# Kernel tuning notes

Measured on AMD Instinct MI355X. Metric: run time of the kernel, lower is better.

The kernel has to match this reference:

```python
import jax, jax.numpy as jnp
import numpy as np


def setup_inputs() -> dict:
    key = jax.random.key(0)
    ks = jax.random.split(key, 7)
    b, c, h, w = 4, 256, 64, 64
    ci = c // 2
    inp = {
        "x0": jax.random.normal(ks[0], (b, 2 * c, h, w), dtype=jnp.float32),
        "x": jax.random.normal(ks[1], (b, c, h, w), dtype=jnp.float32),
        "x_dsm": jax.random.normal(ks[2], (b, c, h, w), dtype=jnp.float32),
        # 1x1 conv weights, stored as [out_ch, in_ch]
        "w_phi": jax.random.normal(ks[3], (ci, c), dtype=jnp.float32) * 0.02,
        "w_theta": jax.random.normal(ks[4], (ci, c), dtype=jnp.float32) * 0.02,
        "w_g": jax.random.normal(ks[5], (c, 2 * c), dtype=jnp.float32) * 0.02,
        "w_mask": jax.random.normal(ks[6], (2 * c, c), dtype=jnp.float32) * 0.02,
    }
    return inp


def reference(x0, x, x_dsm, w_phi, w_theta, w_g, w_mask):
    b, c, h, w = x.shape
    ci = c // 2
    n = h * w
    # 1x1 convs as channel matmuls
    phi = jnp.einsum('oc,bchw->bohw', w_phi, x).reshape(b, ci, n)            # [b, ci, N]
    theta = jnp.einsum('oc,bchw->bohw', w_theta, x_dsm).reshape(b, ci, n)    # [b, ci, N]
    theta = theta.transpose(0, 2, 1)                                         # [b, N, ci]
    g = jnp.einsum('oc,bchw->bohw', w_g, x0).reshape(b, c, n).transpose(0, 2, 1)  # [b, N, c]
    scores = jnp.matmul(theta, phi)                                          # [b, N, N]
    # NOTE: original uses nn.Softmax(dim=1) -> normalize over the FIRST N axis
    attn = jax.nn.softmax(scores, axis=1)
    out = jnp.matmul(attn, g)                                                # [b, N, c]
    out = out.transpose(0, 2, 1).reshape(b, c, h, w)
    mask = jnp.einsum('oc,bchw->bohw', w_mask, out)                          # [b, 2c, h, w]
    return mask + x0
```

## Files before the change

kernel.cpp:

```cpp
#include <hip/hip_runtime.h>
#include <math.h>

#define NB 4
#define NC 256
#define NCI 128
#define NC2 512
#define NPOS 4096
#define ISPLIT 8

using bf16x8 = __attribute__((ext_vector_type(8))) short;
using f32x4  = __attribute__((ext_vector_type(4))) float;

__device__ inline unsigned short f2bf(float f) {
  unsigned int u = __float_as_uint(f);
  u = (u + 0x7fffu + ((u >> 16) & 1u)) >> 16;
  return (unsigned short)u;
}
__device__ inline float bf2f(short s) {
  return __uint_as_float(((unsigned int)(unsigned short)s) << 16);
}

__global__ void k_cast4(const float* __restrict__ s0, short* __restrict__ d0, int n0,
                        const float* __restrict__ s1, short* __restrict__ d1, int n1,
                        const float* __restrict__ s2, short* __restrict__ d2, int n2,
                        const float* __restrict__ s3, short* __restrict__ d3, int n3) {
  int i = blockIdx.x * 256 + threadIdx.x;
  if (i < n0) { d0[i] = (short)f2bf(s0[i]); return; } i -= n0;
  if (i < n1) { d1[i] = (short)f2bf(s1[i]); return; } i -= n1;
  if (i < n2) { d2[i] = (short)f2bf(s2[i]); return; } i -= n2;
  if (i < n3) { d3[i] = (short)f2bf(s3[i]); }
}

__global__ __launch_bounds__(256) void k_tcast(
    const float* __restrict__ in, short* __restrict__ out,
    int R, int C, size_t inBs, size_t outBs) {
  __shared__ float t[64][65];
  const int tid = threadIdx.x;
  const int r0 = blockIdx.y * 64, c0 = blockIdx.x * 64, b = blockIdx.z;
  {
    int r = tid >> 2, cc = (tid & 3) * 16;
    const float* ib = in + (size_t)b * inBs + (size_t)(r0 + r) * C + c0 + cc;
#pragma unroll
    for (int i = 0; i < 4; ++i) {
      float4 v = *(const float4*)(ib + i * 4);
      t[r][cc + i * 4 + 0] = v.x; t[r][cc + i * 4 + 1] = v.y;
      t[r][cc + i * 4 + 2] = v.z; t[r][cc + i * 4 + 3] = v.w;
    }
  }
  __syncthreads();
  {
    int c = tid >> 2, rr = (tid & 3) * 16;
    __align__(16) short v[16];
#pragma unroll
    for (int i = 0; i < 16; ++i) v[i] = (short)f2bf(t[rr + i][c]);
    short* ob = out + (size_t)b * outBs + (size_t)(c0 + c) * R + r0 + rr;
    *(int4*)(ob) = *(const int4*)(v);
    *(int4*)(ob + 8) = *(const int4*)(v + 8);
  }
}

__global__ __launch_bounds__(256) void k_tcast2(
    const float* __restrict__ inA, const float* __restrict__ inB,
    short* __restrict__ out, int R, int C, size_t inBs, size_t outBs) {
  __shared__ float t[64][65];
  const int tid = threadIdx.x;
  const int r0 = blockIdx.y * 64, c0 = blockIdx.x * 64, b = blockIdx.z;
  {
    int r = tid >> 2, cc = (tid & 3) * 16;
    size_t base = (size_t)b * inBs + (size_t)(r0 + r) * C + c0 + cc;
#pragma unroll
    for (int i = 0; i < 4; ++i) {
      float4 va = *(const float4*)(inA + base + i * 4);
      float4 vb = *(const float4*)(inB + base + i * 4);
      t[r][cc + i * 4 + 0] = va.x + vb.x; t[r][cc + i * 4 + 1] = va.y + vb.y;
      t[r][cc + i * 4 + 2] = va.z + vb.z; t[r][cc + i * 4 + 3] = va.w + vb.w;
    }
  }
  __syncthreads();
  {
    int c = tid >> 2, rr = (tid & 3) * 16;
    __align__(16) short v[16];
#pragma unroll
    for (int i = 0; i < 16; ++i) v[i] = (short)f2bf(t[rr + i][c]);
    short* ob = out + (size_t)b * outBs + (size_t)(c0 + c) * R + r0 + rr;
    *(int4*)(ob) = *(const int4*)(v);
    *(int4*)(ob + 8) = *(const int4*)(v + 8);
  }
}

template<bool OUT_BF16, bool HAS_RES>
__global__ __launch_bounds__(256, 2) void k_gemm(
    const short* __restrict__ A, const short* __restrict__ B,
    void* __restrict__ outv, const float* __restrict__ res,
    int K, int sN, size_t aBs, size_t bBs, size_t oBs) {
  __shared__ short As[2][64 * 64];
  __shared__ short Bs_[2][64 * 64];
  const int tid = threadIdx.x, lane = tid & 63, w = tid >> 6;
  const int x = lane & 15, q = lane >> 4;
  const int wm = (w & 1) * 32, wn = (w >> 1) * 32;
  const int n0 = blockIdx.x * 64, m0 = blockIdx.y * 64, b = blockIdx.z;
  const short* Ab = A + (size_t)b * aBs + (size_t)m0 * K;
  const short* Bb = B + (size_t)b * bBs + (size_t)n0 * K;
  const int r = tid >> 2, cth = tid & 3;
  f32x4 acc[2][2];
  acc[0][0] = acc[0][1] = acc[1][0] = acc[1][1] = (f32x4){0.f, 0.f, 0.f, 0.f};
  int4 ra[2], rb[2];
  const int NK = K >> 6;
#define GLOAD(kt)                                                              \
  { _Pragma("unroll") for (int i = 0; i < 2; ++i) {                            \
      ra[i] = *(const int4*)(Ab + (size_t)r * K + (kt) * 64 + (cth + i * 4) * 8); \
      rb[i] = *(const int4*)(Bb + (size_t)r * K + (kt) * 64 + (cth + i * 4) * 8); } }
#define GWRITE(buf)                                                            \
  { _Pragma("unroll") for (int i = 0; i < 2; ++i) {                            \
      *(int4*)(&As[buf][r * 64 + (((cth + i * 4) ^ (r & 7)) * 8)]) = ra[i];    \
      *(int4*)(&Bs_[buf][r * 64 + (((cth + i * 4) ^ (r & 7)) * 8)]) = rb[i]; } }
  GLOAD(0); GWRITE(0); __syncthreads();
  int cur = 0;
  for (int kt = 0; kt < NK; ++kt) {
    if (kt + 1 < NK) GLOAD(kt + 1);
    bf16x8 af[2][2], bfr[2][2];
#pragma unroll
    for (int ms = 0; ms < 2; ++ms) {
      int rowm = wm + ms * 16 + x;
#pragma unroll
      for (int ks = 0; ks < 2; ++ks)
        af[ms][ks] = *(const bf16x8*)(&As[cur][rowm * 64 + (((ks * 4 + q) ^ (rowm & 7)) * 8)]);
    }
#pragma unroll
    for (int ns = 0; ns < 2; ++ns) {
      int rown = wn + ns * 16 + x;
#pragma unroll
      for (int ks = 0; ks < 2; ++ks)
        bfr[ns][ks] = *(const bf16x8*)(&Bs_[cur][rown * 64 + (((ks * 4 + q) ^ (rown & 7)) * 8)]);
    }
#pragma unroll
    for (int ms = 0; ms < 2; ++ms)
#pragma unroll
      for (int ns = 0; ns < 2; ++ns)
#pragma unroll
        for (int ks = 0; ks < 2; ++ks)
          acc[ms][ns] = __builtin_amdgcn_mfma_f32_16x16x32_bf16(
              af[ms][ks], bfr[ns][ks], acc[ms][ns], 0, 0, 0);
    if (kt + 1 < NK) GWRITE(cur ^ 1);
    __syncthreads();
    cur ^= 1;
  }
#pragma unroll
  for (int ms = 0; ms < 2; ++ms)
#pragma unroll
    for (int ns = 0; ns < 2; ++ns) {
      int n = n0 + wn + ns * 16 + x;
      int m = m0 + wm + ms * 16 + q * 4;
      size_t off = (size_t)b * oBs + (size_t)n * sN + m;
      if (OUT_BF16) {
        __align__(8) short pv[4];
#pragma unroll
        for (int j = 0; j < 4; ++j) pv[j] = (short)f2bf(acc[ms][ns][j]);
        *(uint2*)((short*)outv + off) = *(const uint2*)pv;
      } else {
        float4 v = {acc[ms][ns][0], acc[ms][ns][1], acc[ms][ns][2], acc[ms][ns][3]};
        if (HAS_RES) {
          float4 rv = *(const float4*)(res + off);
          v.x += rv.x; v.y += rv.y; v.z += rv.z; v.w += rv.w;
        }
        *(float4*)((float*)outv + off) = v;
      }
    }
#undef GLOAD
#undef GWRITE
}

__global__ __launch_bounds__(256, 4) void k_lsum(
    const short* __restrict__ phiB, const short* __restrict__ thetaB,
    float* __restrict__ plsum) {
  __shared__ short thT[2][64 * 128];
  const int tid = threadIdx.x, lane = tid & 63, w = tid >> 6;
  const int x = lane & 15, q = lane >> 4;
  const int j0 = blockIdx.x * 64, iy = blockIdx.y, b = blockIdx.z;
  const short* phb = phiB + (size_t)b * NPOS * NCI;
  const short* thb = thetaB + (size_t)b * NPOS * NCI + (size_t)iy * (NPOS / ISPLIT) * NCI;
  bf16x8 af[4];
  {
    const short* pr = phb + (size_t)(j0 + w * 16 + x) * NCI;
#pragma unroll
    for (int kk = 0; kk < 4; ++kk) af[kk] = *(const bf16x8*)(pr + kk * 32 + q * 8);
  }
  float lsum[4] = {0.f, 0.f, 0.f, 0.f};
  int4 rt[4];
  const int NIT = NPOS / ISPLIT / 64;
#define LSUM_LOAD(it)                                                         \
  { _Pragma("unroll") for (int r = 0; r < 4; ++r) {                           \
      int s = tid + r * 256; int row = s >> 4, c = s & 15;                    \
      rt[r] = *(const int4*)(thb + (size_t)((it) * 64 + row) * NCI + c * 8); } }
#define LSUM_WRITE(buf)                                                       \
  { _Pragma("unroll") for (int r = 0; r < 4; ++r) {                           \
      int s = tid + r * 256; int row = s >> 4, c = s & 15;                    \
      *(int4*)(&thT[buf][row * 128 + ((c ^ (row & 7)) * 8)]) = rt[r]; } }
  LSUM_LOAD(0); LSUM_WRITE(0); __syncthreads();
  int cur = 0;
  for (int it = 0; it < NIT; ++it) {
    if (it + 1 < NIT) LSUM_LOAD(it + 1);
#pragma unroll
    for (int ii = 0; ii < 4; ++ii) {
      f32x4 s = {0.f, 0.f, 0.f, 0.f};
      int row = ii * 16 + x;
      int sw = row & 7;
#pragma unroll
      for (int kk = 0; kk < 4; ++kk) {
        bf16x8 bfv = *(const bf16x8*)(&thT[cur][row * 128 + (((kk * 4 + q) ^ sw) * 8)]);
        s = __builtin_amdgcn_mfma_f32_16x16x32_bf16(af[kk], bfv, s, 0, 0, 0);
      }
#pragma unroll
      for (int r = 0; r < 4; ++r) lsum[r] += __expf(s[r]);
    }
    if (it + 1 < NIT) LSUM_WRITE(cur ^ 1);
    __syncthreads();
    cur ^= 1;
  }
#pragma unroll
  for (int m = 1; m < 16; m <<= 1)
#pragma unroll
    for (int r = 0; r < 4; ++r) lsum[r] += __shfl_xor(lsum[r], m);
  if (x == 0) {
#pragma unroll
    for (int r = 0; r < 4; ++r)
      plsum[((size_t)(b * ISPLIT + iy) << 12) + j0 + w * 16 + 4 * q + r] = lsum[r];
  }
#undef LSUM_LOAD
#undef LSUM_WRITE
}

__global__ void k_lcomb(const float* __restrict__ plsum, float* __restrict__ linv) {
  int i = blockIdx.x * 256 + threadIdx.x;
  int b = i >> 12, j = i & (NPOS - 1);
  float s = 0.f;
#pragma unroll
  for (int t = 0; t < ISPLIT; ++t) s += plsum[((size_t)(b * ISPLIT + t) << 12) + j];
  linv[i] = 1.0f / s;
}

__global__ void k_scale_g(short* __restrict__ gB, const float* __restrict__ linv) {
  size_t e = ((size_t)blockIdx.x * 256 + threadIdx.x) * 8;
  int b = (int)(e >> 20);
  int p = (int)(e & (NPOS - 1));
  __align__(16) short v[8];
  *(int4*)v = *(const int4*)(gB + e);
  const float* lv = linv + ((size_t)b << 12) + p;
#pragma unroll
  for (int k = 0; k < 8; ++k) v[k] = (short)f2bf(bf2f(v[k]) * lv[k]);
  *(int4*)(gB + e) = *(const int4*)v;
}

__global__ __launch_bounds__(256, 2) void k_attn(
    const short* __restrict__ phiB, const short* __restrict__ thetaB,
    const short* __restrict__ gB, float* __restrict__ omidP) {
  __shared__ short phiT[2][32 * 128];
  __shared__ short gT[2][256 * 32];
  __shared__ short pT[4][16 * 32];
  const int tid = threadIdx.x, lane = tid & 63, w = tid >> 6;
  const int x = lane & 15, q = lane >> 4;
  const int i0 = blockIdx.x * 64, jh = blockIdx.y, b = blockIdx.z;
  const short* phb = phiB + (size_t)b * NPOS * NCI;
  const short* thb = thetaB + (size_t)b * NPOS * NCI;
  const short* gb = gB + (size_t)b * NC * NPOS;
  float* om = omidP + ((size_t)(jh * NB + b)) * NC * NPOS;

  bf16x8 tf[4];
  {
    const short* tr = thb + (size_t)(i0 + w * 16 + x) * NCI;
#pragma unroll
    for (int kk = 0; kk < 4; ++kk) tf[kk] = *(const bf16x8*)(tr + kk * 32 + q * 8);
  }
  f32x4 acc[16];
#pragma unroll
  for (int i = 0; i < 16; ++i) acc[i] = (f32x4){0.f, 0.f, 0.f, 0.f};

  const int sgx = (x & 3) ^ ((x >> 2) & 1);
  int4 rphi[2], rg[4];
  const int NT = 64;
  const int jbase = jh * 64;
#define ATTN_LOAD(jt)                                                          \
  { _Pragma("unroll") for (int r = 0; r < 2; ++r) {                            \
      int s = tid + r * 256; int row = s >> 4, c = s & 15;                     \
      rphi[r] = *(const int4*)(phb + (size_t)((jbase + (jt)) * 32 + row) * NCI + c * 8); } \
    _Pragma("unroll") for (int r = 0; r < 4; ++r) {                            \
      int s = tid + r * 256; int cc = s >> 2, c4 = s & 3;                      \
      rg[r] = *(const int4*)(gb + (size_t)cc * NPOS + (jbase + (jt)) * 32 + c4 * 8); } }
#define ATTN_WRITE(buf)                                                        \
  { _Pragma("unroll") for (int r = 0; r < 2; ++r) {                            \
      int s = tid + r * 256; int row = s >> 4, c = s & 15;                     \
      *(int4*)(&phiT[buf][row * 128 + ((c ^ (row & 7)) * 8)]) = rphi[r]; }     \
    _Pragma("unroll") for (int r = 0; r < 4; ++r) {                            \
      int s = tid + r * 256; int cc = s >> 2, c4 = s & 3;                      \
      int sw = (cc & 3) ^ ((cc >> 2) & 1);                                     \
      *(int4*)(&gT[buf][cc * 32 + ((c4 ^ sw) * 8)]) = rg[r]; } }
  ATTN_LOAD(0); ATTN_WRITE(0); __syncthreads();
  int cur = 0;
  for (int jt = 0; jt < NT; ++jt) {
    if (jt + 1 < NT) ATTN_LOAD(jt + 1);
    {
      const short* PH = &phiT[cur][0];
      const short* GT = &gT[cur][0];
      short* PW = &pT[w][0];
#pragma unroll
      for (int jsub = 0; jsub < 2; ++jsub) {
        f32x4 s = {0.f, 0.f, 0.f, 0.f};
        int row = jsub * 16 + x;
        int sw = row & 7;
#pragma unroll
        for (int kk = 0; kk < 4; ++kk) {
          bf16x8 a = *(const bf16x8*)(PH + row * 128 + (((kk * 4 + q) ^ sw) * 8));
          s = __builtin_amdgcn_mfma_f32_16x16x32_bf16(a, tf[kk], s, 0, 0, 0);
        }
        unsigned short p0 = f2bf(__expf(s[0]));
        unsigned short p1 = f2bf(__expf(s[1]));
        unsigned short p2 = f2bf(__expf(s[2]));
        unsigned short p3 = f2bf(__expf(s[3]));
        unsigned int lo = (unsigned int)p0 | ((unsigned int)p1 << 16);
        unsigned int hi = (unsigned int)p2 | ((unsigned int)p3 << 16);
        int byteoff = (x * 64 + jsub * 32 + q * 8) ^ ((((x >> 1) & 3)) << 4);
        *(uint2*)((char*)PW + byteoff) = make_uint2(lo, hi);
      }
      {
        int c = q ^ ((x >> 1) & 3);
        bf16x8 ap = *(const bf16x8*)((const char*)PW + x * 64 + c * 16);
#pragma unroll
        for (int cf = 0; cf < 16; ++cf) {
          bf16x8 bg = *(const bf16x8*)(GT + (cf * 16 + x) * 32 + ((q ^ sgx) * 8));
          acc[cf] = __builtin_amdgcn_mfma_f32_16x16x32_bf16(ap, bg, acc[cf], 0, 0, 0);
        }
      }
    }
    if (jt + 1 < NT) ATTN_WRITE(cur ^ 1);
    __syncthreads();
    cur ^= 1;
  }
#pragma unroll
  for (int cf = 0; cf < 16; ++cf) {
    size_t o = (size_t)(cf * 16 + x) * NPOS + i0 + w * 16 + 4 * q;
    *reinterpret_cast<f32x4*>(&om[o]) = acc[cf];
  }
#undef ATTN_LOAD
#undef ATTN_WRITE
}

extern "C" void kernel_launch(void* const* d_in, const int* in_sizes, int n_in,
                              void* d_out, int out_size, void* d_ws, size_t ws_size,
                              hipStream_t stream) {
  (void)in_sizes; (void)n_in; (void)out_size; (void)ws_size;
  const float* x0      = (const float*)d_in[0];
  const float* x       = (const float*)d_in[1];
  const float* x_dsm   = (const float*)d_in[2];
  const float* w_phi   = (const float*)d_in[3];
  const float* w_theta = (const float*)d_in[4];
  const float* w_g     = (const float*)d_in[5];
  const float* w_mask  = (const float*)d_in[6];
  float* outp = (float*)d_out;

  short* sp = (short*)d_ws;
  short* wb_phi   = sp; sp += 32768;
  short* wb_theta = sp; sp += 32768;
  short* wb_g     = sp; sp += 131072;
  short* wb_mask  = sp; sp += 131072;
  short* xT   = sp; sp += (size_t)NB * NPOS * NC;
  short* xdT  = sp; sp += (size_t)NB * NPOS * NC;
  short* x0T  = sp; sp += (size_t)NB * NPOS * NC2;
  short* phiB   = sp; sp += (size_t)NB * NPOS * NCI;
  short* thetaB = sp; sp += (size_t)NB * NPOS * NCI;
  short* gBuf   = sp; sp += (size_t)NB * NC * NPOS;
  float* linv = (float*)sp; sp += 2 * (size_t)NB * NPOS;
  float* plsum = (float*)sp;
  float* omidP = (float*)xT;
  short* omidT = phiB;

  k_cast4<<<dim3(1280), 256, 0, stream>>>(w_phi, wb_phi, 32768,
                                          w_theta, wb_theta, 32768,
                                          w_g, wb_g, 131072,
                                          w_mask, wb_mask, 131072);

  k_tcast<<<dim3(64, 4, NB), 256, 0, stream>>>(x, xT, NC, NPOS,
      (size_t)NC * NPOS, (size_t)NPOS * NC);
  k_tcast<<<dim3(64, 4, NB), 256, 0, stream>>>(x_dsm, xdT, NC, NPOS,
      (size_t)NC * NPOS, (size_t)NPOS * NC);
  k_tcast<<<dim3(64, 8, NB), 256, 0, stream>>>(x0, x0T, NC2, NPOS,
      (size_t)NC2 * NPOS, (size_t)NPOS * NC2);

  k_gemm<true, false><<<dim3(64, 2, NB), 256, 0, stream>>>(
      wb_phi, xT, phiB, nullptr, NC, NCI, 0, (size_t)NPOS * NC, (size_t)NPOS * NCI);
  k_gemm<true, false><<<dim3(64, 2, NB), 256, 0, stream>>>(
      wb_theta, xdT, thetaB, nullptr, NC, NCI, 0, (size_t)NPOS * NC, (size_t)NPOS * NCI);
  k_gemm<true, false><<<dim3(4, 64, NB), 256, 0, stream>>>(
      x0T, wb_g, gBuf, nullptr, NC2, NPOS, (size_t)NPOS * NC2, 0, (size_t)NC * NPOS);

  k_lsum<<<dim3(NPOS / 64, ISPLIT, NB), 256, 0, stream>>>(phiB, thetaB, plsum);
  k_lcomb<<<dim3(NB * NPOS / 256), 256, 0, stream>>>(plsum, linv);
  k_scale_g<<<dim3(2048), 256, 0, stream>>>(gBuf, linv);

  k_attn<<<dim3(64, 2, NB), 256, 0, stream>>>(phiB, thetaB, gBuf, omidP);

  k_tcast2<<<dim3(64, 4, NB), 256, 0, stream>>>(omidP, omidP + (size_t)NB * NC * NPOS,
      omidT, NC, NPOS, (size_t)NC * NPOS, (size_t)NPOS * NC);

  k_gemm<false, true><<<dim3(8, 64, NB), 256, 0, stream>>>(
      omidT, wb_mask, outp, x0, NC, NPOS, (size_t)NPOS * NC, 0, (size_t)NC2 * NPOS);
}
```

Before: 255.3 us.

## Retile attention kernel across warps, split keys four ways, store bf16 partials

The attention kernel now has warps split the P computation by key half and query half, then share P through LDS. Each warp owns 64 output channels across all 64 queries, so each g fragment feeds four MFMAs instead of one. The key dimension is split four ways instead of two, which gives more blocks, and occupancy is raised to 3. Partial outputs are written as bf16 instead of fp32 and reduced by a new 4-way transpose-cast kernel. The costs are an extra barrier per tile and bf16 rounding of the partial sums.

```diff
diff --git a/kernel.cpp b/kernel.cpp
--- a/kernel.cpp
+++ b/kernel.cpp
@@ -59,22 +59,25 @@
   }
 }
 
-__global__ __launch_bounds__(256) void k_tcast2(
-    const float* __restrict__ inA, const float* __restrict__ inB,
-    short* __restrict__ out, int R, int C, size_t inBs, size_t outBs) {
+__global__ __launch_bounds__(256) void k_tcast4(
+    const short* __restrict__ inP, short* __restrict__ out) {
   __shared__ float t[64][65];
   const int tid = threadIdx.x;
   const int r0 = blockIdx.y * 64, c0 = blockIdx.x * 64, b = blockIdx.z;
   {
     int r = tid >> 2, cc = (tid & 3) * 16;
-    size_t base = (size_t)b * inBs + (size_t)(r0 + r) * C + c0 + cc;
-#pragma unroll
-    for (int i = 0; i < 4; ++i) {
-      float4 va = *(const float4*)(inA + base + i * 4);
-      float4 vb = *(const float4*)(inB + base + i * 4);
-      t[r][cc + i * 4 + 0] = va.x + vb.x; t[r][cc + i * 4 + 1] = va.y + vb.y;
-      t[r][cc + i * 4 + 2] = va.z + vb.z; t[r][cc + i * 4 + 3] = va.w + vb.w;
-    }
+    float tacc[16] = {};
+#pragma unroll
+    for (int p = 0; p < 4; ++p) {
+      const short* ib = inP + ((size_t)p * NB + b) * NC * NPOS +
+                        (size_t)(r0 + r) * NPOS + c0 + cc;
+      bf16x8 a = *(const bf16x8*)(ib);
+      bf16x8 a2 = *(const bf16x8*)(ib + 8);
+#pragma unroll
+      for (int i = 0; i < 8; ++i) { tacc[i] += bf2f(a[i]); tacc[8 + i] += bf2f(a2[i]); }
+    }
+#pragma unroll
+    for (int i = 0; i < 16; ++i) t[r][cc + i] = tacc[i];
   }
   __syncthreads();
   {
@@ -82,7 +85,7 @@
     __align__(16) short v[16];
 #pragma unroll
     for (int i = 0; i < 16; ++i) v[i] = (short)f2bf(t[rr + i][c]);
-    short* ob = out + (size_t)b * outBs + (size_t)(c0 + c) * R + r0 + rr;
+    short* ob = out + (size_t)b * (size_t)NPOS * NC + (size_t)(c0 + c) * NC + r0 + rr;
     *(int4*)(ob) = *(const int4*)(v);
     *(int4*)(ob + 8) = *(const int4*)(v + 8);
   }
@@ -251,41 +254,46 @@
   *(int4*)(gB + e) = *(const int4*)v;
 }
 
-__global__ __launch_bounds__(256, 2) void k_attn(
+__global__ __launch_bounds__(256, 3) void k_attn(
     const short* __restrict__ phiB, const short* __restrict__ thetaB,
-    const short* __restrict__ gB, float* __restrict__ omidP) {
+    const short* __restrict__ gB, short* __restrict__ omidP) {
   __shared__ short phiT[2][32 * 128];
   __shared__ short gT[2][256 * 32];
-  __shared__ short pT[4][16 * 32];
+  __shared__ short pT[64 * 32];
   const int tid = threadIdx.x, lane = tid & 63, w = tid >> 6;
   const int x = lane & 15, q = lane >> 4;
-  const int i0 = blockIdx.x * 64, jh = blockIdx.y, b = blockIdx.z;
+  const int jsub = w & 1, ih = w >> 1;
+  const int i0 = blockIdx.x * 64, jq = blockIdx.y, b = blockIdx.z;
   const short* phb = phiB + (size_t)b * NPOS * NCI;
   const short* thb = thetaB + (size_t)b * NPOS * NCI;
   const short* gb = gB + (size_t)b * NC * NPOS;
-  float* om = omidP + ((size_t)(jh * NB + b)) * NC * NPOS;
-
-  bf16x8 tf[4];
-  {
-    const short* tr = thb + (size_t)(i0 + w * 16 + x) * NCI;
-#pragma unroll
-    for (int kk = 0; kk < 4; ++kk) tf[kk] = *(const bf16x8*)(tr + kk * 32 + q * 8);
-  }
-  f32x4 acc[16];
-#pragma unroll
-  for (int i = 0; i < 16; ++i) acc[i] = (f32x4){0.f, 0.f, 0.f, 0.f};
-
+  short* om = omidP + ((size_t)(jq * NB + b)) * NC * NPOS;
+
+  bf16x8 tf[2][4];
+#pragma unroll
+  for (int f = 0; f < 2; ++f) {
+    const short* tr = thb + (size_t)(i0 + ih * 32 + f * 16 + x) * NCI;
+#pragma unroll
+    for (int kk = 0; kk < 4; ++kk) tf[f][kk] = *(const bf16x8*)(tr + kk * 32 + q * 8);
+  }
+  f32x4 acc[4][4];
+#pragma unroll
+  for (int i = 0; i < 4; ++i)
+#pragma unroll
+    for (int j = 0; j < 4; ++j) acc[i][j] = (f32x4){0.f, 0.f, 0.f, 0.f};
+
+  const int sx = (x >> 1) & 3;
   const int sgx = (x & 3) ^ ((x >> 2) & 1);
   int4 rphi[2], rg[4];
-  const int NT = 64;
-  const int jbase = jh * 64;
+  const int NT = 32;
+  const int JT0 = jq * 32;
 #define ATTN_LOAD(jt)                                                          \
   { _Pragma("unroll") for (int r = 0; r < 2; ++r) {                            \
       int s = tid + r * 256; int row = s >> 4, c = s & 15;                     \
-      rphi[r] = *(const int4*)(phb + (size_t)((jbase + (jt)) * 32 + row) * NCI + c * 8); } \
+      rphi[r] = *(const int4*)(phb + (size_t)((JT0 + (jt)) * 32 + row) * NCI + c * 8); } \
     _Pragma("unroll") for (int r = 0; r < 4; ++r) {                            \
       int s = tid + r * 256; int cc = s >> 2, c4 = s & 3;                      \
-      rg[r] = *(const int4*)(gb + (size_t)cc * NPOS + (jbase + (jt)) * 32 + c4 * 8); } }
+      rg[r] = *(const int4*)(gb + (size_t)cc * NPOS + (JT0 + (jt)) * 32 + c4 * 8); } }
 #define ATTN_WRITE(buf)                                                        \
   { _Pragma("unroll") for (int r = 0; r < 2; ++r) {                            \
       int s = tid + r * 256; int row = s >> 4, c = s & 15;                     \
@@ -298,19 +306,18 @@
   int cur = 0;
   for (int jt = 0; jt < NT; ++jt) {
     if (jt + 1 < NT) ATTN_LOAD(jt + 1);
+    const short* PH = &phiT[cur][0];
+    const short* GT = &gT[cur][0];
     {
-      const short* PH = &phiT[cur][0];
-      const short* GT = &gT[cur][0];
-      short* PW = &pT[w][0];
-#pragma unroll
-      for (int jsub = 0; jsub < 2; ++jsub) {
+      int row = jsub * 16 + x;
+      int swr = row & 7;
+#pragma unroll
+      for (int f = 0; f < 2; ++f) {
         f32x4 s = {0.f, 0.f, 0.f, 0.f};
-        int row = jsub * 16 + x;
-        int sw = row & 7;
 #pragma unroll
         for (int kk = 0; kk < 4; ++kk) {
-          bf16x8 a = *(const bf16x8*)(PH + row * 128 + (((kk * 4 + q) ^ sw) * 8));
-          s = __builtin_amdgcn_mfma_f32_16x16x32_bf16(a, tf[kk], s, 0, 0, 0);
+          bf16x8 a = *(const bf16x8*)(PH + row * 128 + (((kk * 4 + q) ^ swr) * 8));
+          s = __builtin_amdgcn_mfma_f32_16x16x32_bf16(a, tf[f][kk], s, 0, 0, 0);
         }
         unsigned short p0 = f2bf(__expf(s[0]));
         unsigned short p1 = f2bf(__expf(s[1]));
@@ -318,17 +325,24 @@
         unsigned short p3 = f2bf(__expf(s[3]));
         unsigned int lo = (unsigned int)p0 | ((unsigned int)p1 << 16);
         unsigned int hi = (unsigned int)p2 | ((unsigned int)p3 << 16);
-        int byteoff = (x * 64 + jsub * 32 + q * 8) ^ ((((x >> 1) & 3)) << 4);
-        *(uint2*)((char*)PW + byteoff) = make_uint2(lo, hi);
+        int irow = ih * 32 + f * 16 + x;
+        int byteoff = (irow * 64 + jsub * 32 + q * 8) ^ (sx << 4);
+        *(uint2*)((char*)pT + byteoff) = make_uint2(lo, hi);
       }
-      {
-        int c = q ^ ((x >> 1) & 3);
-        bf16x8 ap = *(const bf16x8*)((const char*)PW + x * 64 + c * 16);
-#pragma unroll
-        for (int cf = 0; cf < 16; ++cf) {
-          bf16x8 bg = *(const bf16x8*)(GT + (cf * 16 + x) * 32 + ((q ^ sgx) * 8));
-          acc[cf] = __builtin_amdgcn_mfma_f32_16x16x32_bf16(ap, bg, acc[cf], 0, 0, 0);
-        }
+    }
+    __syncthreads();
+    {
+      bf16x8 ap[4];
+#pragma unroll
+      for (int f = 0; f < 4; ++f)
+        ap[f] = *(const bf16x8*)((const char*)pT + (f * 16 + x) * 64 + ((q ^ sx) * 16));
+#pragma unroll
+      for (int cfl = 0; cfl < 4; ++cfl) {
+        int row = w * 64 + cfl * 16 + x;
+        bf16x8 bg = *(const bf16x8*)(GT + row * 32 + ((q ^ sgx) * 8));
+#pragma unroll
+        for (int f = 0; f < 4; ++f)
+          acc[f][cfl] = __builtin_amdgcn_mfma_f32_16x16x32_bf16(ap[f], bg, acc[f][cfl], 0, 0, 0);
       }
     }
     if (jt + 1 < NT) ATTN_WRITE(cur ^ 1);
@@ -336,10 +350,15 @@
     cur ^= 1;
   }
 #pragma unroll
-  for (int cf = 0; cf < 16; ++cf) {
-    size_t o = (size_t)(cf * 16 + x) * NPOS + i0 + w * 16 + 4 * q;
-    *reinterpret_cast<f32x4*>(&om[o]) = acc[cf];
-  }
+  for (int f = 0; f < 4; ++f)
+#pragma unroll
+    for (int cfl = 0; cfl < 4; ++cfl) {
+      __align__(8) short pv[4];
+#pragma unroll
+      for (int j = 0; j < 4; ++j) pv[j] = (short)f2bf(acc[f][cfl][j]);
+      size_t o = (size_t)(w * 64 + cfl * 16 + x) * NPOS + i0 + f * 16 + 4 * q;
+      *(uint2*)(om + o) = *(const uint2*)pv;
+    }
 #undef ATTN_LOAD
 #undef ATTN_WRITE
 }
@@ -370,7 +389,7 @@
   short* gBuf   = sp; sp += (size_t)NB * NC * NPOS;
   float* linv = (float*)sp; sp += 2 * (size_t)NB * NPOS;
   float* plsum = (float*)sp;
-  float* omidP = (float*)xT;
+  short* omidP = xT;
   short* omidT = phiB;
 
   k_cast4<<<dim3(1280), 256, 0, stream>>>(w_phi, wb_phi, 32768,
@@ -396,10 +415,9 @@
   k_lcomb<<<dim3(NB * NPOS / 256), 256, 0, stream>>>(plsum, linv);
   k_scale_g<<<dim3(2048), 256, 0, stream>>>(gBuf, linv);
 
-  k_attn<<<dim3(64, 2, NB), 256, 0, stream>>>(phiB, thetaB, gBuf, omidP);
-
-  k_tcast2<<<dim3(64, 4, NB), 256, 0, stream>>>(omidP, omidP + (size_t)NB * NC * NPOS,
-      omidT, NC, NPOS, (size_t)NC * NPOS, (size_t)NPOS * NC);
+  k_attn<<<dim3(64, 4, NB), 256, 0, stream>>>(phiB, thetaB, gBuf, omidP);
+
+  k_tcast4<<<dim3(64, 4, NB), 256, 0, stream>>>(omidP, omidT);
 
   k_gemm<false, true><<<dim3(8, 64, NB), 256, 0, stream>>>(
       omidT, wb_mask, outp, x0, NC, NPOS, (size_t)NPOS * NC, 0, (size_t)NC2 * NPOS);
```

After: 427.9 us. +67.6%, slower.

## Fuse softmax normalization into attention, share P tile across waves, bf16 partials

Applied to the files above, without the earlier changes.

Merges the three input transpose-cast launches into one kernel and removes the separate g-scaling pass by multiplying exp(scores) by the column inverse sums inside the attention kernel. The attention kernel now writes all four waves' P tiles into one shared tile, synchronizes, and has each wave compute a 64x64 output block (4x4 MFMA tiles), so each g fragment is reused across four P fragments instead of one. Partial outputs are stored as bf16 rather than fp32, which halves the write and read traffic into the transpose-add kernel. The cost is an extra barrier per j-tile, extra linv loads in the inner loop, and reduced precision of the partial sums.

```diff
diff --git a/kernel.cpp b/kernel.cpp
--- a/kernel.cpp
+++ b/kernel.cpp
@@ -31,15 +31,21 @@
   if (i < n3) { d3[i] = (short)f2bf(s3[i]); }
 }
 
-__global__ __launch_bounds__(256) void k_tcast(
-    const float* __restrict__ in, short* __restrict__ out,
-    int R, int C, size_t inBs, size_t outBs) {
+__global__ __launch_bounds__(256) void k_tcast_all(
+    const float* __restrict__ x, const float* __restrict__ xdsm,
+    const float* __restrict__ x0, short* __restrict__ xT,
+    short* __restrict__ xdT, short* __restrict__ x0T) {
   __shared__ float t[64][65];
   const int tid = threadIdx.x;
-  const int r0 = blockIdx.y * 64, c0 = blockIdx.x * 64, b = blockIdx.z;
+  const int y = blockIdx.y, c0 = blockIdx.x * 64, b = blockIdx.z;
+  const float* in; short* out; int R, r0;
+  if (y < 4)      { in = x;    out = xT;  R = NC;  r0 = y * 64; }
+  else if (y < 8) { in = xdsm; out = xdT; R = NC;  r0 = (y - 4) * 64; }
+  else            { in = x0;   out = x0T; R = NC2; r0 = (y - 8) * 64; }
+  const size_t inBs = (size_t)R * NPOS, outBs = (size_t)NPOS * R;
   {
     int r = tid >> 2, cc = (tid & 3) * 16;
-    const float* ib = in + (size_t)b * inBs + (size_t)(r0 + r) * C + c0 + cc;
+    const float* ib = in + (size_t)b * inBs + (size_t)(r0 + r) * NPOS + c0 + cc;
 #pragma unroll
     for (int i = 0; i < 4; ++i) {
       float4 v = *(const float4*)(ib + i * 4);
@@ -60,20 +66,22 @@
 }
 
 __global__ __launch_bounds__(256) void k_tcast2(
-    const float* __restrict__ inA, const float* __restrict__ inB,
-    short* __restrict__ out, int R, int C, size_t inBs, size_t outBs) {
+    const short* __restrict__ inA, const short* __restrict__ inB,
+    short* __restrict__ out) {
   __shared__ float t[64][65];
   const int tid = threadIdx.x;
   const int r0 = blockIdx.y * 64, c0 = blockIdx.x * 64, b = blockIdx.z;
   {
     int r = tid >> 2, cc = (tid & 3) * 16;
-    size_t base = (size_t)b * inBs + (size_t)(r0 + r) * C + c0 + cc;
-#pragma unroll
-    for (int i = 0; i < 4; ++i) {
-      float4 va = *(const float4*)(inA + base + i * 4);
-      float4 vb = *(const float4*)(inB + base + i * 4);
-      t[r][cc + i * 4 + 0] = va.x + vb.x; t[r][cc + i * 4 + 1] = va.y + vb.y;
-      t[r][cc + i * 4 + 2] = va.z + vb.z; t[r][cc + i * 4 + 3] = va.w + vb.w;
+    size_t base = (size_t)b * NC * NPOS + (size_t)(r0 + r) * NPOS + c0 + cc;
+    bf16x8 a0 = *(const bf16x8*)(inA + base);
+    bf16x8 a1 = *(const bf16x8*)(inA + base + 8);
+    bf16x8 b0 = *(const bf16x8*)(inB + base);
+    bf16x8 b1 = *(const bf16x8*)(inB + base + 8);
+#pragma unroll
+    for (int i = 0; i < 8; ++i) {
+      t[r][cc + i] = bf2f(a0[i]) + bf2f(b0[i]);
+      t[r][cc + 8 + i] = bf2f(a1[i]) + bf2f(b1[i]);
     }
   }
   __syncthreads();
@@ -82,7 +90,7 @@
     __align__(16) short v[16];
 #pragma unroll
     for (int i = 0; i < 16; ++i) v[i] = (short)f2bf(t[rr + i][c]);
-    short* ob = out + (size_t)b * outBs + (size_t)(c0 + c) * R + r0 + rr;
+    short* ob = out + (size_t)b * (size_t)NPOS * NC + (size_t)(c0 + c) * NC + r0 + rr;
     *(int4*)(ob) = *(const int4*)(v);
     *(int4*)(ob + 8) = *(const int4*)(v + 8);
   }
@@ -239,31 +247,21 @@
   linv[i] = 1.0f / s;
 }
 
-__global__ void k_scale_g(short* __restrict__ gB, const float* __restrict__ linv) {
-  size_t e = ((size_t)blockIdx.x * 256 + threadIdx.x) * 8;
-  int b = (int)(e >> 20);
-  int p = (int)(e & (NPOS - 1));
-  __align__(16) short v[8];
-  *(int4*)v = *(const int4*)(gB + e);
-  const float* lv = linv + ((size_t)b << 12) + p;
-#pragma unroll
-  for (int k = 0; k < 8; ++k) v[k] = (short)f2bf(bf2f(v[k]) * lv[k]);
-  *(int4*)(gB + e) = *(const int4*)v;
-}
-
 __global__ __launch_bounds__(256, 2) void k_attn(
     const short* __restrict__ phiB, const short* __restrict__ thetaB,
-    const short* __restrict__ gB, float* __restrict__ omidP) {
+    const short* __restrict__ gB, const float* __restrict__ linv,
+    short* __restrict__ omidP) {
   __shared__ short phiT[2][32 * 128];
   __shared__ short gT[2][256 * 32];
-  __shared__ short pT[4][16 * 32];
+  __shared__ short pT[64 * 32];
   const int tid = threadIdx.x, lane = tid & 63, w = tid >> 6;
   const int x = lane & 15, q = lane >> 4;
   const int i0 = blockIdx.x * 64, jh = blockIdx.y, b = blockIdx.z;
   const short* phb = phiB + (size_t)b * NPOS * NCI;
   const short* thb = thetaB + (size_t)b * NPOS * NCI;
   const short* gb = gB + (size_t)b * NC * NPOS;
-  float* om = omidP + ((size_t)(jh * NB + b)) * NC * NPOS;
+  const float* lvb = linv + ((size_t)b << 12);
+  short* om = omidP + ((size_t)(jh * NB + b)) * NC * NPOS;
 
   bf16x8 tf[4];
   {
@@ -271,10 +269,13 @@
 #pragma unroll
     for (int kk = 0; kk < 4; ++kk) tf[kk] = *(const bf16x8*)(tr + kk * 32 + q * 8);
   }
-  f32x4 acc[16];
-#pragma unroll
-  for (int i = 0; i < 16; ++i) acc[i] = (f32x4){0.f, 0.f, 0.f, 0.f};
-
+  f32x4 acc[4][4];
+#pragma unroll
+  for (int i = 0; i < 4; ++i)
+#pragma unroll
+    for (int j = 0; j < 4; ++j) acc[i][j] = (f32x4){0.f, 0.f, 0.f, 0.f};
+
+  const int px = (x >> 1) & 3;
   const int sgx = (x & 3) ^ ((x >> 2) & 1);
   int4 rphi[2], rg[4];
   const int NT = 64;
@@ -300,8 +301,6 @@
     if (jt + 1 < NT) ATTN_LOAD(jt + 1);
     {
       const short* PH = &phiT[cur][0];
-      const short* GT = &gT[cur][0];
-      short* PW = &pT[w][0];
 #pragma unroll
       for (int jsub = 0; jsub < 2; ++jsub) {
         f32x4 s = {0.f, 0.f, 0.f, 0.f};
@@ -312,23 +311,32 @@
           bf16x8 a = *(const bf16x8*)(PH + row * 128 + (((kk * 4 + q) ^ sw) * 8));
           s = __builtin_amdgcn_mfma_f32_16x16x32_bf16(a, tf[kk], s, 0, 0, 0);
         }
-        unsigned short p0 = f2bf(__expf(s[0]));
-        unsigned short p1 = f2bf(__expf(s[1]));
-        unsigned short p2 = f2bf(__expf(s[2]));
-        unsigned short p3 = f2bf(__expf(s[3]));
+        float4 lv = *(const float4*)(lvb + (jbase + jt) * 32 + jsub * 16 + 4 * q);
+        unsigned short p0 = f2bf(__expf(s[0]) * lv.x);
+        unsigned short p1 = f2bf(__expf(s[1]) * lv.y);
+        unsigned short p2 = f2bf(__expf(s[2]) * lv.z);
+        unsigned short p3 = f2bf(__expf(s[3]) * lv.w);
         unsigned int lo = (unsigned int)p0 | ((unsigned int)p1 << 16);
         unsigned int hi = (unsigned int)p2 | ((unsigned int)p3 << 16);
-        int byteoff = (x * 64 + jsub * 32 + q * 8) ^ ((((x >> 1) & 3)) << 4);
-        *(uint2*)((char*)PW + byteoff) = make_uint2(lo, hi);
+        int irow = w * 16 + x;
+        int byteoff = (irow * 64 + jsub * 32 + q * 8) ^ (px << 4);
+        *(uint2*)((char*)pT + byteoff) = make_uint2(lo, hi);
       }
-      {
-        int c = q ^ ((x >> 1) & 3);
-        bf16x8 ap = *(const bf16x8*)((const char*)PW + x * 64 + c * 16);
-#pragma unroll
-        for (int cf = 0; cf < 16; ++cf) {
-          bf16x8 bg = *(const bf16x8*)(GT + (cf * 16 + x) * 32 + ((q ^ sgx) * 8));
-          acc[cf] = __builtin_amdgcn_mfma_f32_16x16x32_bf16(ap, bg, acc[cf], 0, 0, 0);
-        }
+    }
+    __syncthreads();
+    {
+      const short* GT = &gT[cur][0];
+      bf16x8 ap[4];
+#pragma unroll
+      for (int f = 0; f < 4; ++f)
+        ap[f] = *(const bf16x8*)((const char*)pT + (f * 16 + x) * 64 + ((q ^ px) << 4));
+#pragma unroll
+      for (int cl = 0; cl < 4; ++cl) {
+        int grow = w * 64 + cl * 16 + x;
+        bf16x8 bg = *(const bf16x8*)(GT + grow * 32 + ((q ^ sgx) * 8));
+#pragma unroll
+        for (int f = 0; f < 4; ++f)
+          acc[f][cl] = __builtin_amdgcn_mfma_f32_16x16x32_bf16(ap[f], bg, acc[f][cl], 0, 0, 0);
       }
     }
     if (jt + 1 < NT) ATTN_WRITE(cur ^ 1);
@@ -336,10 +344,15 @@
     cur ^= 1;
   }
 #pragma unroll
-  for (int cf = 0; cf < 16; ++cf) {
-    size_t o = (size_t)(cf * 16 + x) * NPOS + i0 + w * 16 + 4 * q;
-    *reinterpret_cast<f32x4*>(&om[o]) = acc[cf];
-  }
+  for (int f = 0; f < 4; ++f)
+#pragma unroll
+    for (int cl = 0; cl < 4; ++cl) {
+      __align__(8) short pv[4];
+#pragma unroll
+      for (int j = 0; j < 4; ++j) pv[j] = (short)f2bf(acc[f][cl][j]);
+      size_t o = (size_t)(w * 64 + cl * 16 + x) * NPOS + i0 + f * 16 + 4 * q;
+      *(uint2*)(om + o) = *(const uint2*)pv;
+    }
 #undef ATTN_LOAD
 #undef ATTN_WRITE
 }
@@ -370,7 +383,7 @@
   short* gBuf   = sp; sp += (size_t)NB * NC * NPOS;
   float* linv = (float*)sp; sp += 2 * (size_t)NB * NPOS;
   float* plsum = (float*)sp;
-  float* omidP = (float*)xT;
+  short* omidP = xT;
   short* omidT = phiB;
 
   k_cast4<<<dim3(1280), 256, 0, stream>>>(w_phi, wb_phi, 32768,
@@ -378,12 +391,7 @@
                                           w_g, wb_g, 131072,
                                           w_mask, wb_mask, 131072);
 
-  k_tcast<<<dim3(64, 4, NB), 256, 0, stream>>>(x, xT, NC, NPOS,
-      (size_t)NC * NPOS, (size_t)NPOS * NC);
-  k_tcast<<<dim3(64, 4, NB), 256, 0, stream>>>(x_dsm, xdT, NC, NPOS,
-      (size_t)NC * NPOS, (size_t)NPOS * NC);
-  k_tcast<<<dim3(64, 8, NB), 256, 0, stream>>>(x0, x0T, NC2, NPOS,
-      (size_t)NC2 * NPOS, (size_t)NPOS * NC2);
+  k_tcast_all<<<dim3(64, 16, NB), 256, 0, stream>>>(x, x_dsm, x0, xT, xdT, x0T);
 
   k_gemm<true, false><<<dim3(64, 2, NB), 256, 0, stream>>>(
       wb_phi, xT, phiB, nullptr, NC, NCI, 0, (size_t)NPOS * NC, (size_t)NPOS * NCI);
@@ -394,12 +402,11 @@
 
   k_lsum<<<dim3(NPOS / 64, ISPLIT, NB), 256, 0, stream>>>(phiB, thetaB, plsum);
   k_lcomb<<<dim3(NB * NPOS / 256), 256, 0, stream>>>(plsum, linv);
-  k_scale_g<<<dim3(2048), 256, 0, stream>>>(gBuf, linv);
-
-  k_attn<<<dim3(64, 2, NB), 256, 0, stream>>>(phiB, thetaB, gBuf, omidP);
-
-  k_tcast2<<<dim3(64, 4, NB), 256, 0, stream>>>(omidP, omidP + (size_t)NB * NC * NPOS,
-      omidT, NC, NPOS, (size_t)NC * NPOS, (size_t)NPOS * NC);
+
+  k_attn<<<dim3(64, 2, NB), 256, 0, stream>>>(phiB, thetaB, gBuf, linv, omidP);
+
+  k_tcast2<<<dim3(64, 4, NB), 256, 0, stream>>>(
+      omidP, omidP + (size_t)NB * NC * NPOS, omidT);
 
   k_gemm<false, true><<<dim3(8, 64, NB), 256, 0, stream>>>(
       omidT, wb_mask, outp, x0, NC, NPOS, (size_t)NPOS * NC, 0, (size_t)NC2 * NPOS);
```

Result: slower. 454.0 us (+77.8%).

## Split attention key range four ways with bf16 partials and fuse input transposes

Applied to the files above, without the earlier changes.

The attention kernel now splits the key dimension into four chunks instead of two, doubling the grid and raising launch bounds to three blocks per CU. Partial outputs are stored in bf16 rather than fp32, and a new combine kernel sums the four partials before transposing. The three input transpose-casts are merged into one launch. This aims to improve CU occupancy and cut launch and partial-write traffic, at some cost in precision of the partial sums.

```diff
diff --git a/kernel.cpp b/kernel.cpp
--- a/kernel.cpp
+++ b/kernel.cpp
@@ -31,15 +31,21 @@
   if (i < n3) { d3[i] = (short)f2bf(s3[i]); }
 }
 
-__global__ __launch_bounds__(256) void k_tcast(
-    const float* __restrict__ in, short* __restrict__ out,
-    int R, int C, size_t inBs, size_t outBs) {
+__global__ __launch_bounds__(256) void k_tcast_all(
+    const float* __restrict__ x, const float* __restrict__ xdsm,
+    const float* __restrict__ x0, short* __restrict__ xT,
+    short* __restrict__ xdT, short* __restrict__ x0T) {
   __shared__ float t[64][65];
   const int tid = threadIdx.x;
-  const int r0 = blockIdx.y * 64, c0 = blockIdx.x * 64, b = blockIdx.z;
+  const int y = blockIdx.y, c0 = blockIdx.x * 64, b = blockIdx.z;
+  const float* in; short* out; int R, r0;
+  if (y < 4)      { in = x;    out = xT;  R = NC;  r0 = y * 64; }
+  else if (y < 8) { in = xdsm; out = xdT; R = NC;  r0 = (y - 4) * 64; }
+  else            { in = x0;   out = x0T; R = NC2; r0 = (y - 8) * 64; }
+  const size_t inBs = (size_t)R * NPOS, outBs = (size_t)NPOS * R;
   {
     int r = tid >> 2, cc = (tid & 3) * 16;
-    const float* ib = in + (size_t)b * inBs + (size_t)(r0 + r) * C + c0 + cc;
+    const float* ib = in + (size_t)b * inBs + (size_t)(r0 + r) * NPOS + c0 + cc;
 #pragma unroll
     for (int i = 0; i < 4; ++i) {
       float4 v = *(const float4*)(ib + i * 4);
@@ -59,22 +65,25 @@
   }
 }
 
-__global__ __launch_bounds__(256) void k_tcast2(
-    const float* __restrict__ inA, const float* __restrict__ inB,
-    short* __restrict__ out, int R, int C, size_t inBs, size_t outBs) {
+__global__ __launch_bounds__(256) void k_tcast4(
+    const short* __restrict__ inP, short* __restrict__ out) {
   __shared__ float t[64][65];
   const int tid = threadIdx.x;
   const int r0 = blockIdx.y * 64, c0 = blockIdx.x * 64, b = blockIdx.z;
   {
     int r = tid >> 2, cc = (tid & 3) * 16;
-    size_t base = (size_t)b * inBs + (size_t)(r0 + r) * C + c0 + cc;
-#pragma unroll
-    for (int i = 0; i < 4; ++i) {
-      float4 va = *(const float4*)(inA + base + i * 4);
-      float4 vb = *(const float4*)(inB + base + i * 4);
-      t[r][cc + i * 4 + 0] = va.x + vb.x; t[r][cc + i * 4 + 1] = va.y + vb.y;
-      t[r][cc + i * 4 + 2] = va.z + vb.z; t[r][cc + i * 4 + 3] = va.w + vb.w;
-    }
+    float tacc[16] = {};
+#pragma unroll
+    for (int p = 0; p < 4; ++p) {
+      const short* ib = inP + ((size_t)p * NB + b) * NC * NPOS +
+                        (size_t)(r0 + r) * NPOS + c0 + cc;
+      bf16x8 a = *(const bf16x8*)(ib);
+      bf16x8 a2 = *(const bf16x8*)(ib + 8);
+#pragma unroll
+      for (int i = 0; i < 8; ++i) { tacc[i] += bf2f(a[i]); tacc[8 + i] += bf2f(a2[i]); }
+    }
+#pragma unroll
+    for (int i = 0; i < 16; ++i) t[r][cc + i] = tacc[i];
   }
   __syncthreads();
   {
@@ -82,7 +91,7 @@
     __align__(16) short v[16];
 #pragma unroll
     for (int i = 0; i < 16; ++i) v[i] = (short)f2bf(t[rr + i][c]);
-    short* ob = out + (size_t)b * outBs + (size_t)(c0 + c) * R + r0 + rr;
+    short* ob = out + (size_t)b * (size_t)NPOS * NC + (size_t)(c0 + c) * NC + r0 + rr;
     *(int4*)(ob) = *(const int4*)(v);
     *(int4*)(ob + 8) = *(const int4*)(v + 8);
   }
@@ -251,19 +260,19 @@
   *(int4*)(gB + e) = *(const int4*)v;
 }
 
-__global__ __launch_bounds__(256, 2) void k_attn(
+__global__ __launch_bounds__(256, 3) void k_attn(
     const short* __restrict__ phiB, const short* __restrict__ thetaB,
-    const short* __restrict__ gB, float* __restrict__ omidP) {
+    const short* __restrict__ gB, short* __restrict__ omidP) {
   __shared__ short phiT[2][32 * 128];
   __shared__ short gT[2][256 * 32];
   __shared__ short pT[4][16 * 32];
   const int tid = threadIdx.x, lane = tid & 63, w = tid >> 6;
   const int x = lane & 15, q = lane >> 4;
-  const int i0 = blockIdx.x * 64, jh = blockIdx.y, b = blockIdx.z;
+  const int i0 = blockIdx.x * 64, jq = blockIdx.y, b = blockIdx.z;
   const short* phb = phiB + (size_t)b * NPOS * NCI;
   const short* thb = thetaB + (size_t)b * NPOS * NCI;
   const short* gb = gB + (size_t)b * NC * NPOS;
-  float* om = omidP + ((size_t)(jh * NB + b)) * NC * NPOS;
+  short* om = omidP + ((size_t)(jq * NB + b)) * NC * NPOS;
 
   bf16x8 tf[4];
   {
@@ -277,8 +286,8 @@
 
   const int sgx = (x & 3) ^ ((x >> 2) & 1);
   int4 rphi[2], rg[4];
-  const int NT = 64;
-  const int jbase = jh * 64;
+  const int NT = 32;
+  const int jbase = jq * 32;
 #define ATTN_LOAD(jt)                                                          \
   { _Pragma("unroll") for (int r = 0; r < 2; ++r) {                            \
       int s = tid + r * 256; int row = s >> 4, c = s & 15;                     \
@@ -337,8 +346,11 @@
   }
 #pragma unroll
   for (int cf = 0; cf < 16; ++cf) {
+    __align__(8) short pv[4];
+#pragma unroll
+    for (int j = 0; j < 4; ++j) pv[j] = (short)f2bf(acc[cf][j]);
     size_t o = (size_t)(cf * 16 + x) * NPOS + i0 + w * 16 + 4 * q;
-    *reinterpret_cast<f32x4*>(&om[o]) = acc[cf];
+    *(uint2*)(om + o) = *(const uint2*)pv;
   }
 #undef ATTN_LOAD
 #undef ATTN_WRITE
@@ -370,7 +382,7 @@
   short* gBuf   = sp; sp += (size_t)NB * NC * NPOS;
   float* linv = (float*)sp; sp += 2 * (size_t)NB * NPOS;
   float* plsum = (float*)sp;
-  float* omidP = (float*)xT;
+  short* omidP = xT;
   short* omidT = phiB;
 
   k_cast4<<<dim3(1280), 256, 0, stream>>>(w_phi, wb_phi, 32768,
@@ -378,12 +390,7 @@
                                           w_g, wb_g, 131072,
                                           w_mask, wb_mask, 131072);
 
-  k_tcast<<<dim3(64, 4, NB), 256, 0, stream>>>(x, xT, NC, NPOS,
-      (size_t)NC * NPOS, (size_t)NPOS * NC);
-  k_tcast<<<dim3(64, 4, NB), 256, 0, stream>>>(x_dsm, xdT, NC, NPOS,
-      (size_t)NC * NPOS, (size_t)NPOS * NC);
-  k_tcast<<<dim3(64, 8, NB), 256, 0, stream>>>(x0, x0T, NC2, NPOS,
-      (size_t)NC2 * NPOS, (size_t)NPOS * NC2);
+  k_tcast_all<<<dim3(64, 16, NB), 256, 0, stream>>>(x, x_dsm, x0, xT, xdT, x0T);
 
   k_gemm<true, false><<<dim3(64, 2, NB), 256, 0, stream>>>(
       wb_phi, xT, phiB, nullptr, NC, NCI, 0, (size_t)NPOS * NC, (size_t)NPOS * NCI);
@@ -396,10 +403,9 @@
   k_lcomb<<<dim3(NB * NPOS / 256), 256, 0, stream>>>(plsum, linv);
   k_scale_g<<<dim3(2048), 256, 0, stream>>>(gBuf, linv);
 
-  k_attn<<<dim3(64, 2, NB), 256, 0, stream>>>(phiB, thetaB, gBuf, omidP);
-
-  k_tcast2<<<dim3(64, 4, NB), 256, 0, stream>>>(omidP, omidP + (size_t)NB * NC * NPOS,
-      omidT, NC, NPOS, (size_t)NC * NPOS, (size_t)NPOS * NC);
+  k_attn<<<dim3(64, 4, NB), 256, 0, stream>>>(phiB, thetaB, gBuf, omidP);
+
+  k_tcast4<<<dim3(64, 4, NB), 256, 0, stream>>>(omidP, omidT);
 
   k_gemm<false, true><<<dim3(8, 64, NB), 256, 0, stream>>>(
       omidT, wb_mask, outp, x0, NC, NPOS, (size_t)NPOS * NC, 0, (size_t)NC2 * NPOS);
```

Result: no change. 251.9 us (-1.3%).
